# Kernel optimization log

Measured on AMD Instinct MI355X. Metric: run time of the kernel, lower is better.

The kernel has to match this reference:

```python
import jax, jax.numpy as jnp
import numpy as np

EMBED = 768
NH = 12          # num_heads
NL = 3           # num_levels
NP = 4           # num_points
DV = 384         # value dim = embed_dim * deform_ratio(0.5)
DH = DV // NH    # per-head value dim = 32
B = 16
LQ = 1024        # (512/16)^2 ViT tokens
SHAPES = [(64, 64), (32, 32), (16, 16)]  # 1/8, 1/16, 1/32 pyramid of 512x512
LKV = sum(h * w for h, w in SHAPES)      # 5376
EPS = 1e-6


def layer_norm(x, w, b):
    mu = jnp.mean(x, axis=-1, keepdims=True)
    var = jnp.mean((x - mu) ** 2, axis=-1, keepdims=True)
    return (x - mu) / jnp.sqrt(var + EPS) * w + b


def bilinear_sample(v, loc, H, W):
    # v: (B, NH, H*W, DH); loc: (B, Lq, NH, P, 2) normalized in [0,1]
    # Matches torch grid_sample(align_corners=False, padding_mode='zeros').
    Bv, Lq = loc.shape[0], loc.shape[1]
    x = loc[..., 0] * W - 0.5
    y = loc[..., 1] * H - 0.5
    x0 = jnp.floor(x)
    y0 = jnp.floor(y)
    dx = x - x0
    dy = y - y0
    x0i = x0.astype(jnp.int32)
    y0i = y0.astype(jnp.int32)

    def gather(xi, yi):
        valid = (xi >= 0) & (xi < W) & (yi >= 0) & (yi < H)  # (B,Lq,NH,P)
        xc = jnp.clip(xi, 0, W - 1)
        yc = jnp.clip(yi, 0, H - 1)
        lin = (yc * W + xc).transpose(0, 2, 1, 3).reshape(Bv, NH, Lq * NP)
        g = jnp.take_along_axis(v, lin[..., None], axis=2)  # (B,NH,Lq*P,DH)
        g = g.reshape(Bv, NH, Lq, NP, DH).transpose(0, 2, 1, 3, 4)  # (B,Lq,NH,P,DH)
        return g * valid[..., None].astype(g.dtype)

    g00 = gather(x0i, y0i)
    g01 = gather(x0i + 1, y0i)
    g10 = gather(x0i, y0i + 1)
    g11 = gather(x0i + 1, y0i + 1)
    w00 = ((1 - dx) * (1 - dy))[..., None]
    w01 = (dx * (1 - dy))[..., None]
    w10 = ((1 - dx) * dy)[..., None]
    w11 = (dx * dy)[..., None]
    return g00 * w00 + g01 * w01 + g10 * w10 + g11 * w11


def ms_deform_attn_core(value, shapes_list, loc, aw):
    # value: (B,LKV,NH,DH); loc: (B,Lq,NH,NL,NP,2); aw: (B,Lq,NH,NL,NP)
    Bv, Lq = loc.shape[0], loc.shape[1]
    samples = []
    idx = 0
    for l, (H, W) in enumerate(shapes_list):
        v = value[:, idx:idx + H * W].transpose(0, 2, 1, 3)  # (B,NH,HW,DH)
        idx += H * W
        samples.append(bilinear_sample(v, loc[:, :, :, l], H, W))
    s = jnp.stack(samples, axis=3)  # (B,Lq,NH,NL,NP,DH)
    o = jnp.einsum('bqhlp,bqhlpd->bqhd', aw, s)
    return o.reshape(Bv, Lq, NH * DH)


def setup_inputs() -> dict:
    key = jax.random.key(0)
    ks = jax.random.split(key, 12)

    def n(k, shape, s=0.02):
        return jax.random.normal(k, shape, jnp.float32) * s

    return {
        'q': jax.random.normal(ks[0], (B, LQ, EMBED), jnp.float32),
        'reference_points': jax.random.uniform(ks[1], (B, LQ, NL, 2), jnp.float32),
        'kv': jax.random.normal(ks[2], (B, LKV, EMBED), jnp.float32),
        'spatial_shapes': jnp.asarray(SHAPES, jnp.int32),
        'level_start_index': jnp.asarray(
            np.cumsum([0] + [h * w for h, w in SHAPES])[:-1], jnp.int32),
        'ln1_w': jnp.ones(EMBED, jnp.float32),
        'ln1_b': jnp.zeros(EMBED, jnp.float32),
        'ln2_w': jnp.ones(EMBED, jnp.float32),
        'ln2_b': jnp.zeros(EMBED, jnp.float32),
        'gamma': n(ks[3], (EMBED,), 0.1),
        'w_off': n(ks[4], (EMBED, NH * NL * NP * 2)),
        'b_off': n(ks[5], (NH * NL * NP * 2,), 0.01),
        'w_aw': n(ks[6], (EMBED, NH * NL * NP)),
        'b_aw': jnp.zeros(NH * NL * NP, jnp.float32),
        'w_val': n(ks[7], (EMBED, DV)),
        'b_val': jnp.zeros(DV, jnp.float32),
        'w_out': n(ks[8], (DV, EMBED)),
        'b_out': jnp.zeros(EMBED, jnp.float32),
    }


def reference(q, reference_points, kv, spatial_shapes, level_start_index,
              ln1_w, ln1_b, ln2_w, ln2_b, gamma,
              w_off, b_off, w_aw, b_aw, w_val, b_val, w_out, b_out):
    shapes_list = [tuple(int(v) for v in r) for r in np.asarray(spatial_shapes)]
    Bq, Lq, _ = q.shape
    qn = layer_norm(q, ln1_w, ln1_b)
    kvn = layer_norm(kv, ln2_w, ln2_b)
    value = (kvn @ w_val + b_val).reshape(Bq, -1, NH, DH)
    off = (qn @ w_off + b_off).reshape(Bq, Lq, NH, NL, NP, 2)
    aw = (qn @ w_aw + b_aw).reshape(Bq, Lq, NH, NL * NP)
    aw = jax.nn.softmax(aw, axis=-1).reshape(Bq, Lq, NH, NL, NP)
    # offset normalizer is (W_l, H_l) per level
    wh = jnp.asarray([[w, h] for (h, w) in shapes_list], q.dtype)  # (NL,2)
    loc = reference_points[:, :, None, :, None, :] + off / wh[None, None, None, :, None, :]
    attn = ms_deform_attn_core(value, shapes_list, loc, aw)
    attn = attn @ w_out + b_out
    return q + gamma * attn
```

## Files before the change

### kernel.cpp

```cpp
#include <hip/hip_runtime.h>

#define DEV __device__ __forceinline__

typedef short bf16x8 __attribute__((ext_vector_type(8)));
typedef float f32x4 __attribute__((ext_vector_type(4)));
typedef unsigned int u32;
typedef __attribute__((address_space(1))) const u32* gas_ptr;
typedef __attribute__((address_space(3))) u32* las_ptr;

DEV short f2bf(float f) {
  union { float f; unsigned u; } un; un.f = f;
  unsigned r = un.u + 0x7FFFu + ((un.u >> 16) & 1u);
  return (short)(r >> 16);
}
DEV float bf2f(unsigned short s) {
  union { unsigned u; float f; } un;
  un.u = ((unsigned)s) << 16;
  return un.f;
}
DEV void gload16(const short* g, short* l) {
  __builtin_amdgcn_global_load_lds((gas_ptr)g, (las_ptr)l, 16, 0, 0);
}

DEV float blockReduceSum256(float v, volatile float* sbuf) {
  #pragma unroll
  for (int off = 32; off > 0; off >>= 1) v += __shfl_down(v, off, 64);
  const int wv = threadIdx.x >> 6, ln = threadIdx.x & 63;
  if (ln == 0) sbuf[wv] = v;
  __syncthreads();
  return sbuf[0] + sbuf[1] + sbuf[2] + sbuf[3];
}

__global__ __launch_bounds__(256) void pack_weights_kernel(
    const float* __restrict__ w_val, const float* __restrict__ w_off,
    const float* __restrict__ w_aw, const float* __restrict__ w_out,
    const float* __restrict__ b_off, const float* __restrict__ b_aw,
    short* __restrict__ wT_val, short* __restrict__ wT_offaw,
    short* __restrict__ wT_out, float* __restrict__ bias_cat) {
  int gid = blockIdx.x * 256 + threadIdx.x;
  const int S0 = 768 * 384, S1 = 768 * 288, S2 = 768 * 144, S3 = 384 * 768;
  const int S4 = 16 * 768, S5 = 448;
  if (gid < S0) { int k = gid / 384, n = gid % 384; wT_val[n * 768 + k] = f2bf(w_val[gid]); return; }
  gid -= S0;
  if (gid < S1) { int k = gid / 288, n = gid % 288; wT_offaw[n * 768 + k] = f2bf(w_off[gid]); return; }
  gid -= S1;
  if (gid < S2) { int k = gid / 144, n = gid % 144; wT_offaw[(288 + n) * 768 + k] = f2bf(w_aw[gid]); return; }
  gid -= S2;
  if (gid < S3) { int k = gid / 768, n = gid % 768; wT_out[n * 384 + k] = f2bf(w_out[gid]); return; }
  gid -= S3;
  if (gid < S4) { wT_offaw[432 * 768 + gid] = 0; return; }
  gid -= S4;
  if (gid < S5) { bias_cat[gid] = (gid < 288) ? b_off[gid] : (gid < 432 ? b_aw[gid - 288] : 0.f); }
}

__global__ __launch_bounds__(256) void ln_norm_kernel(
    const float* __restrict__ x, const float* __restrict__ w,
    const float* __restrict__ b, short* __restrict__ y) {
  const int row = blockIdx.x;
  const float* xr = x + (size_t)row * 768;
  const int t = threadIdx.x;
  float a0 = xr[t], a1 = xr[t + 256], a2 = xr[t + 512];
  __shared__ float sb1[4], sb2[4];
  float mu = blockReduceSum256(a0 + a1 + a2, sb1) * (1.f / 768.f);
  float d0 = a0 - mu, d1 = a1 - mu, d2 = a2 - mu;
  float var = blockReduceSum256(d0 * d0 + d1 * d1 + d2 * d2, sb2) * (1.f / 768.f);
  const float rs = rsqrtf(var + 1e-6f);
  short* yr = y + (size_t)row * 768;
  yr[t]       = f2bf(d0 * rs * w[t]       + b[t]);
  yr[t + 256] = f2bf(d1 * rs * w[t + 256] + b[t + 256]);
  yr[t + 512] = f2bf(d2 * rs * w[t + 512] + b[t + 512]);
}

template <int EMODE>
__global__ __launch_bounds__(256, 3) void gemm128_kernel(
    const short* __restrict__ A, const short* __restrict__ Wt,
    const float* __restrict__ bias, const float* __restrict__ qres,
    const float* __restrict__ gamma, void* __restrict__ Cout,
    const int N, const int K) {
  __shared__ __align__(16) short As[128 * 32];
  __shared__ __align__(16) short Bs[128 * 32];
  const int tid = threadIdx.x;
  const int wave = tid >> 6, lane = tid & 63;
  const int n0 = blockIdx.x * 128, row0 = blockIdx.y * 128;
  const int lr = lane & 15, quad = lane >> 4;
  const int wm = wave >> 1, wn = wave & 1;

  const short* gA[2]; const short* gB[2];
  #pragma unroll
  for (int rnd = 0; rnd < 2; rnd++) {
    int G = rnd * 256 + wave * 64 + lane;
    int line = G >> 3, pos = G & 7, x = pos ^ (line & 7);
    int r = line * 2 + (x >> 2), qk = (x & 3) * 8;
    gA[rnd] = A + (size_t)(row0 + r) * K + qk;
    gB[rnd] = Wt + (size_t)(n0 + r) * K + qk;
  }
  short* ldsA[2] = {&As[(wave * 64) * 8], &As[(256 + wave * 64) * 8]};
  short* ldsB[2] = {&Bs[(wave * 64) * 8], &Bs[(256 + wave * 64) * 8]};

  const short* aF[4]; const short* bF[4];
  #pragma unroll
  for (int t4 = 0; t4 < 4; t4++) {
    int r = wm * 64 + t4 * 16 + lr;
    int line = r >> 1, pos = ((r & 1) * 4 + quad) ^ (line & 7);
    aF[t4] = &As[(line * 8 + pos) * 8];
    int rb = wn * 64 + t4 * 16 + lr;
    int lineb = rb >> 1, posb = ((rb & 1) * 4 + quad) ^ (lineb & 7);
    bF[t4] = &Bs[(lineb * 8 + posb) * 8];
  }

  f32x4 acc[4][4];
  #pragma unroll
  for (int i = 0; i < 4; i++)
    #pragma unroll
    for (int j = 0; j < 4; j++)
      #pragma unroll
      for (int e = 0; e < 4; e++) acc[i][j][e] = 0.f;

  for (int k0 = 0; k0 < K; k0 += 32) {
    gload16(gA[0], ldsA[0]);
    gload16(gA[1], ldsA[1]);
    gload16(gB[0], ldsB[0]);
    gload16(gB[1], ldsB[1]);
    gA[0] += 32; gA[1] += 32; gB[0] += 32; gB[1] += 32;
    __syncthreads();
    bf16x8 av[4], bv[4];
    #pragma unroll
    for (int t4 = 0; t4 < 4; t4++) {
      av[t4] = *(const bf16x8*)aF[t4];
      bv[t4] = *(const bf16x8*)bF[t4];
    }
    #pragma unroll
    for (int ct = 0; ct < 4; ct++)
      #pragma unroll
      for (int rt = 0; rt < 4; rt++)
        acc[rt][ct] = __builtin_amdgcn_mfma_f32_16x16x32_bf16(av[rt], bv[ct], acc[rt][ct], 0, 0, 0);
    __syncthreads();
  }

  #pragma unroll
  for (int ct = 0; ct < 4; ct++) {
    const int n = n0 + wn * 64 + ct * 16 + lr;
    const float bs = bias[n];
    const float gm = (EMODE == 2) ? gamma[n] : 0.f;
    #pragma unroll
    for (int rt = 0; rt < 4; rt++) {
      #pragma unroll
      for (int i = 0; i < 4; i++) {
        const int m = row0 + wm * 64 + rt * 16 + quad * 4 + i;
        float v = acc[rt][ct][i] + bs;
        if (EMODE == 0) {
          ((short*)Cout)[(size_t)m * N + n] = f2bf(v);
        } else {
          ((float*)Cout)[(size_t)m * N + n] = qres[(size_t)m * N + n] + gm * v;
        }
      }
    }
  }
}

template <int NT2>
__global__ __launch_bounds__(256, 2) void gemmw_kernel(
    const short* __restrict__ A, const short* __restrict__ Wt,
    const float* __restrict__ bias, float* __restrict__ Cout,
    const int N, const int K) {
  constexpr int BN = NT2 * 64;
  __shared__ __align__(16) short As[64 * 40];
  __shared__ __align__(16) short Bs[BN * 40];
  const int tid = threadIdx.x;
  const int wave = tid >> 6, lane = tid & 63;
  const int sr = tid >> 2;
  const int sk = (tid & 3) * 8;
  const int n0 = blockIdx.x * BN;
  const int row0 = blockIdx.y * 64;
  const int lr = lane & 15, quad = lane >> 4;

  f32x4 acc[4][NT2];
  #pragma unroll
  for (int rt = 0; rt < 4; rt++)
    #pragma unroll
    for (int cb = 0; cb < NT2; cb++)
      #pragma unroll
      for (int j = 0; j < 4; j++) acc[rt][cb][j] = 0.f;

  const short* AsF = &As[lr * 40 + quad * 8];
  const short* BsF = &Bs[(wave * NT2 * 16 + lr) * 40 + quad * 8];

  for (int k0 = 0; k0 < K; k0 += 32) {
    bf16x8 av = *(const bf16x8*)(A + (size_t)(row0 + sr) * K + k0 + sk);
    *(bf16x8*)(&As[sr * 40 + sk]) = av;
    #pragma unroll
    for (int i = tid; i < BN * 4; i += 256) {
      int n = i >> 2, kk = (i & 3) * 8;
      *(bf16x8*)(&Bs[n * 40 + kk]) =
          *(const bf16x8*)(Wt + (size_t)(n0 + n) * K + k0 + kk);
    }
    __syncthreads();
    bf16x8 af[4];
    #pragma unroll
    for (int rt = 0; rt < 4; rt++) af[rt] = *(const bf16x8*)(AsF + rt * 16 * 40);
    #pragma unroll
    for (int cb = 0; cb < NT2; cb++) {
      bf16x8 bfv = *(const bf16x8*)(BsF + cb * 16 * 40);
      #pragma unroll
      for (int rt = 0; rt < 4; rt++)
        acc[rt][cb] = __builtin_amdgcn_mfma_f32_16x16x32_bf16(af[rt], bfv, acc[rt][cb], 0, 0, 0);
    }
    __syncthreads();
  }

  #pragma unroll
  for (int cb = 0; cb < NT2; cb++) {
    const int n = n0 + wave * NT2 * 16 + cb * 16 + lr;
    const float bs = bias[n];
    #pragma unroll
    for (int rt = 0; rt < 4; rt++) {
      #pragma unroll
      for (int i = 0; i < 4; i++) {
        const int m = row0 + rt * 16 + quad * 4 + i;
        Cout[(size_t)m * N + n] = acc[rt][cb][i] + bs;
      }
    }
  }
}

__global__ __launch_bounds__(384) void sampler_kernel(
    const float* __restrict__ offaw,
    const float* __restrict__ refp,
    const short* __restrict__ value,
    short* __restrict__ o) {
  const int tid = threadIdx.x;
  const int qi = tid / 96, t = tid % 96;
  const int head = t >> 3, ln4 = t & 7;
  const int bq = blockIdx.x * 4 + qi;
  __shared__ __align__(16) float s[4][440];
  __shared__ float sref[4][6];
  const float* row = offaw + (size_t)bq * 448;
  #pragma unroll
  for (int i = t; i < 108; i += 96)
    *(float4*)&s[qi][i * 4] = *(const float4*)&row[i * 4];
  if (t < 6) sref[qi][t] = refp[(size_t)bq * 6 + t];
  __syncthreads();

  const float* awp = &s[qi][288 + head * 12];
  float mx = awp[0];
  #pragma unroll
  for (int j = 1; j < 12; j++) mx = fmaxf(mx, awp[j]);
  float wgt[12];
  float ssum = 0.f;
  #pragma unroll
  for (int j = 0; j < 12; j++) { float e = __expf(awp[j] - mx); wgt[j] = e; ssum += e; }
  const float inv = 1.f / ssum;

  const int b = bq >> 10;
  const unsigned short* vb =
      (const unsigned short*)value + (size_t)b * 5376 * 384 + head * 32 + ln4 * 4;
  float4 acc = make_float4(0.f, 0.f, 0.f, 0.f);
  const int HW[3] = {64, 32, 16};
  const int starts[3] = {0, 4096, 5120};
  #pragma unroll
  for (int l = 0; l < 3; l++) {
    const int Wi = HW[l];
    const float Wf = (float)Wi;
    const float rx = sref[qi][l * 2], ry = sref[qi][l * 2 + 1];
    const unsigned short* base = vb + (size_t)starts[l] * 384;
    #pragma unroll
    for (int p = 0; p < 4; p++) {
      const int oi = ((head * 3 + l) * 4 + p) * 2;
      float x = fmaf(rx, Wf, s[qi][oi] - 0.5f);
      float y = fmaf(ry, Wf, s[qi][oi + 1] - 0.5f);
      float xf = floorf(x), yf = floorf(y);
      float dx = x - xf, dy = y - yf;
      int x0 = (int)xf, y0 = (int)yf;
      int x1 = x0 + 1, y1 = y0 + 1;
      int x0c = min(max(x0, 0), Wi - 1), x1c = min(max(x1, 0), Wi - 1);
      int y0c = min(max(y0, 0), Wi - 1), y1c = min(max(y1, 0), Wi - 1);
      float wx0 = (x0 >= 0 && x0 < Wi) ? (1.f - dx) : 0.f;
      float wx1 = (x1 < Wi && x1 >= 0) ? dx : 0.f;
      float wy0 = (y0 >= 0 && y0 < Wi) ? (1.f - dy) : 0.f;
      float wy1 = (y1 < Wi && y1 >= 0) ? dy : 0.f;
      const ushort4 u00 = *(const ushort4*)(base + (size_t)(y0c * Wi + x0c) * 384);
      const ushort4 u01 = *(const ushort4*)(base + (size_t)(y0c * Wi + x1c) * 384);
      const ushort4 u10 = *(const ushort4*)(base + (size_t)(y1c * Wi + x0c) * 384);
      const ushort4 u11 = *(const ushort4*)(base + (size_t)(y1c * Wi + x1c) * 384);
      const float w00 = wx0 * wy0, w01 = wx1 * wy0, w10 = wx0 * wy1, w11 = wx1 * wy1;
      const float g = wgt[l * 4 + p];
      acc.x += g * (w00 * bf2f(u00.x) + w01 * bf2f(u01.x) + w10 * bf2f(u10.x) + w11 * bf2f(u11.x));
      acc.y += g * (w00 * bf2f(u00.y) + w01 * bf2f(u01.y) + w10 * bf2f(u10.y) + w11 * bf2f(u11.y));
      acc.z += g * (w00 * bf2f(u00.z) + w01 * bf2f(u01.z) + w10 * bf2f(u10.z) + w11 * bf2f(u11.z));
      acc.w += g * (w00 * bf2f(u00.w) + w01 * bf2f(u01.w) + w10 * bf2f(u10.w) + w11 * bf2f(u11.w));
    }
  }
  ushort4 outv;
  outv.x = (unsigned short)f2bf(acc.x * inv);
  outv.y = (unsigned short)f2bf(acc.y * inv);
  outv.z = (unsigned short)f2bf(acc.z * inv);
  outv.w = (unsigned short)f2bf(acc.w * inv);
  *(ushort4*)((unsigned short*)o + (size_t)bq * 384 + head * 32 + ln4 * 4) = outv;
}

extern "C" void kernel_launch(void* const* d_in, const int* in_sizes, int n_in,
                              void* d_out, int out_size, void* d_ws, size_t ws_size,
                              hipStream_t stream) {
  (void)in_sizes; (void)n_in; (void)out_size; (void)ws_size;
  const float* q     = (const float*)d_in[0];
  const float* refp  = (const float*)d_in[1];
  const float* kv    = (const float*)d_in[2];
  const float* ln1w  = (const float*)d_in[5];
  const float* ln1b  = (const float*)d_in[6];
  const float* ln2w  = (const float*)d_in[7];
  const float* ln2b  = (const float*)d_in[8];
  const float* gamma = (const float*)d_in[9];
  const float* w_off = (const float*)d_in[10];
  const float* b_off = (const float*)d_in[11];
  const float* w_aw  = (const float*)d_in[12];
  const float* b_aw  = (const float*)d_in[13];
  const float* w_val = (const float*)d_in[14];
  const float* b_val = (const float*)d_in[15];
  const float* w_out = (const float*)d_in[16];
  const float* b_out = (const float*)d_in[17];
  float* out = (float*)d_out;

  char* wsp = (char*)d_ws;
  size_t cur = 0;
  auto alloc = [&](size_t bytes) -> void* {
    cur = (cur + 255) & ~(size_t)255;
    void* p = wsp + cur;
    cur += bytes;
    return p;
  };
  short*  wT_val   = (short*)alloc((size_t)384 * 768 * 2);
  short*  wT_offaw = (short*)alloc((size_t)448 * 768 * 2);
  short*  wT_out   = (short*)alloc((size_t)768 * 384 * 2);
  float*  bias_cat = (float*)alloc((size_t)448 * 4);
  short*  kvn      = (short*)alloc((size_t)86016 * 768 * 2);
  short*  qn       = (short*)alloc((size_t)16384 * 768 * 2);
  short*  value    = (short*)alloc((size_t)86016 * 384 * 2);
  float*  offaw    = (float*)alloc((size_t)16384 * 448 * 4);
  short*  obuf     = (short*)alloc((size_t)16384 * 384 * 2);

  pack_weights_kernel<<<3651, 256, 0, stream>>>(w_val, w_off, w_aw, w_out, b_off,
                                                b_aw, wT_val, wT_offaw, wT_out,
                                                bias_cat);
  ln_norm_kernel<<<86016, 256, 0, stream>>>(kv, ln2w, ln2b, kvn);
  ln_norm_kernel<<<16384, 256, 0, stream>>>(q, ln1w, ln1b, qn);
  gemm128_kernel<0><<<dim3(3, 672), 256, 0, stream>>>(
      kvn, wT_val, b_val, nullptr, nullptr, value, 384, 768);
  gemmw_kernel<7><<<dim3(1, 256), 256, 0, stream>>>(
      qn, wT_offaw, bias_cat, offaw, 448, 768);
  sampler_kernel<<<4096, 384, 0, stream>>>(offaw, refp, value, obuf);
  gemm128_kernel<2><<<dim3(6, 128), 256, 0, stream>>>(
      obuf, wT_out, b_out, q, gamma, out, 768, 384);
}
```

Measured before the change: 735.9 us.

## Use wave-per-row LayerNorm, swizzle GEMM blocks, pad offaw GEMM to 512 columns

LayerNorm now gives each row to a single wave, loading with float4 and reducing with xor shuffles, which removes the LDS round trips and block barriers. The GEMM kernel remaps block IDs into 8 interleaved groups so neighbouring blocks land on different XCDs or caches. The offset/attention-weight projection is padded from 448 to 512 columns so it can reuse the 128x128 GEMM in place of the separate narrow-tile kernel. The padding adds some wasted MFMA work and a larger intermediate buffer.

```diff
diff --git a/kernel.cpp b/kernel.cpp
--- a/kernel.cpp
+++ b/kernel.cpp
@@ -21,15 +21,7 @@
 DEV void gload16(const short* g, short* l) {
   __builtin_amdgcn_global_load_lds((gas_ptr)g, (las_ptr)l, 16, 0, 0);
 }
-
-DEV float blockReduceSum256(float v, volatile float* sbuf) {
-  #pragma unroll
-  for (int off = 32; off > 0; off >>= 1) v += __shfl_down(v, off, 64);
-  const int wv = threadIdx.x >> 6, ln = threadIdx.x & 63;
-  if (ln == 0) sbuf[wv] = v;
-  __syncthreads();
-  return sbuf[0] + sbuf[1] + sbuf[2] + sbuf[3];
-}
+DEV float hsum4(float4 v) { return v.x + v.y + v.z + v.w; }
 
 __global__ __launch_bounds__(256) void pack_weights_kernel(
     const float* __restrict__ w_val, const float* __restrict__ w_off,
@@ -39,7 +31,7 @@
     short* __restrict__ wT_out, float* __restrict__ bias_cat) {
   int gid = blockIdx.x * 256 + threadIdx.x;
   const int S0 = 768 * 384, S1 = 768 * 288, S2 = 768 * 144, S3 = 384 * 768;
-  const int S4 = 16 * 768, S5 = 448;
+  const int S4 = 80 * 768, S5 = 512;
   if (gid < S0) { int k = gid / 384, n = gid % 384; wT_val[n * 768 + k] = f2bf(w_val[gid]); return; }
   gid -= S0;
   if (gid < S1) { int k = gid / 288, n = gid % 288; wT_offaw[n * 768 + k] = f2bf(w_off[gid]); return; }
@@ -53,22 +45,51 @@
   if (gid < S5) { bias_cat[gid] = (gid < 288) ? b_off[gid] : (gid < 432 ? b_aw[gid - 288] : 0.f); }
 }
 
-__global__ __launch_bounds__(256) void ln_norm_kernel(
+__global__ __launch_bounds__(256) void ln_norm4_kernel(
     const float* __restrict__ x, const float* __restrict__ w,
     const float* __restrict__ b, short* __restrict__ y) {
-  const int row = blockIdx.x;
+  const int wv = threadIdx.x >> 6, lane = threadIdx.x & 63;
+  const int row = blockIdx.x * 4 + wv;
   const float* xr = x + (size_t)row * 768;
-  const int t = threadIdx.x;
-  float a0 = xr[t], a1 = xr[t + 256], a2 = xr[t + 512];
-  __shared__ float sb1[4], sb2[4];
-  float mu = blockReduceSum256(a0 + a1 + a2, sb1) * (1.f / 768.f);
-  float d0 = a0 - mu, d1 = a1 - mu, d2 = a2 - mu;
-  float var = blockReduceSum256(d0 * d0 + d1 * d1 + d2 * d2, sb2) * (1.f / 768.f);
-  const float rs = rsqrtf(var + 1e-6f);
-  short* yr = y + (size_t)row * 768;
-  yr[t]       = f2bf(d0 * rs * w[t]       + b[t]);
-  yr[t + 256] = f2bf(d1 * rs * w[t + 256] + b[t + 256]);
-  yr[t + 512] = f2bf(d2 * rs * w[t + 512] + b[t + 512]);
+  float4 v0 = *(const float4*)(xr + lane * 4);
+  float4 v1 = *(const float4*)(xr + 256 + lane * 4);
+  float4 v2 = *(const float4*)(xr + 512 + lane * 4);
+  float s = hsum4(v0) + hsum4(v1) + hsum4(v2);
+  #pragma unroll
+  for (int off = 32; off > 0; off >>= 1) s += __shfl_xor(s, off, 64);
+  const float mu = s * (1.f / 768.f);
+  float4 d0 = make_float4(v0.x - mu, v0.y - mu, v0.z - mu, v0.w - mu);
+  float4 d1 = make_float4(v1.x - mu, v1.y - mu, v1.z - mu, v1.w - mu);
+  float4 d2 = make_float4(v2.x - mu, v2.y - mu, v2.z - mu, v2.w - mu);
+  float vs = d0.x * d0.x + d0.y * d0.y + d0.z * d0.z + d0.w * d0.w +
+             d1.x * d1.x + d1.y * d1.y + d1.z * d1.z + d1.w * d1.w +
+             d2.x * d2.x + d2.y * d2.y + d2.z * d2.z + d2.w * d2.w;
+  #pragma unroll
+  for (int off = 32; off > 0; off >>= 1) vs += __shfl_xor(vs, off, 64);
+  const float rs = rsqrtf(vs * (1.f / 768.f) + 1e-6f);
+  const float4 w0 = *(const float4*)(w + lane * 4);
+  const float4 w1 = *(const float4*)(w + 256 + lane * 4);
+  const float4 w2 = *(const float4*)(w + 512 + lane * 4);
+  const float4 b0 = *(const float4*)(b + lane * 4);
+  const float4 b1 = *(const float4*)(b + 256 + lane * 4);
+  const float4 b2 = *(const float4*)(b + 512 + lane * 4);
+  unsigned short* yr = (unsigned short*)y + (size_t)row * 768;
+  ushort4 o;
+  o.x = (unsigned short)f2bf(d0.x * rs * w0.x + b0.x);
+  o.y = (unsigned short)f2bf(d0.y * rs * w0.y + b0.y);
+  o.z = (unsigned short)f2bf(d0.z * rs * w0.z + b0.z);
+  o.w = (unsigned short)f2bf(d0.w * rs * w0.w + b0.w);
+  *(ushort4*)(yr + lane * 4) = o;
+  o.x = (unsigned short)f2bf(d1.x * rs * w1.x + b1.x);
+  o.y = (unsigned short)f2bf(d1.y * rs * w1.y + b1.y);
+  o.z = (unsigned short)f2bf(d1.z * rs * w1.z + b1.z);
+  o.w = (unsigned short)f2bf(d1.w * rs * w1.w + b1.w);
+  *(ushort4*)(yr + 256 + lane * 4) = o;
+  o.x = (unsigned short)f2bf(d2.x * rs * w2.x + b2.x);
+  o.y = (unsigned short)f2bf(d2.y * rs * w2.y + b2.y);
+  o.z = (unsigned short)f2bf(d2.z * rs * w2.z + b2.z);
+  o.w = (unsigned short)f2bf(d2.w * rs * w2.w + b2.w);
+  *(ushort4*)(yr + 512 + lane * 4) = o;
 }
 
 template <int EMODE>
@@ -81,7 +102,13 @@
   __shared__ __align__(16) short Bs[128 * 32];
   const int tid = threadIdx.x;
   const int wave = tid >> 6, lane = tid & 63;
-  const int n0 = blockIdx.x * 128, row0 = blockIdx.y * 128;
+
+  const int nx = gridDim.x;
+  const int id = blockIdx.y * nx + blockIdx.x;
+  const int cpx = (nx * gridDim.y) >> 3;
+  const int swz = (id & 7) * cpx + (id >> 3);
+  const int n0 = (swz % nx) * 128, row0 = (swz / nx) * 128;
+
   const int lr = lane & 15, quad = lane >> 4;
   const int wm = wave >> 1, wn = wave & 1;
 
@@ -150,74 +177,11 @@
         float v = acc[rt][ct][i] + bs;
         if (EMODE == 0) {
           ((short*)Cout)[(size_t)m * N + n] = f2bf(v);
+        } else if (EMODE == 1) {
+          ((float*)Cout)[(size_t)m * N + n] = v;
         } else {
           ((float*)Cout)[(size_t)m * N + n] = qres[(size_t)m * N + n] + gm * v;
         }
-      }
-    }
-  }
-}
-
-template <int NT2>
-__global__ __launch_bounds__(256, 2) void gemmw_kernel(
-    const short* __restrict__ A, const short* __restrict__ Wt,
-    const float* __restrict__ bias, float* __restrict__ Cout,
-    const int N, const int K) {
-  constexpr int BN = NT2 * 64;
-  __shared__ __align__(16) short As[64 * 40];
-  __shared__ __align__(16) short Bs[BN * 40];
-  const int tid = threadIdx.x;
-  const int wave = tid >> 6, lane = tid & 63;
-  const int sr = tid >> 2;
-  const int sk = (tid & 3) * 8;
-  const int n0 = blockIdx.x * BN;
-  const int row0 = blockIdx.y * 64;
-  const int lr = lane & 15, quad = lane >> 4;
-
-  f32x4 acc[4][NT2];
-  #pragma unroll
-  for (int rt = 0; rt < 4; rt++)
-    #pragma unroll
-    for (int cb = 0; cb < NT2; cb++)
-      #pragma unroll
-      for (int j = 0; j < 4; j++) acc[rt][cb][j] = 0.f;
-
-  const short* AsF = &As[lr * 40 + quad * 8];
-  const short* BsF = &Bs[(wave * NT2 * 16 + lr) * 40 + quad * 8];
-
-  for (int k0 = 0; k0 < K; k0 += 32) {
-    bf16x8 av = *(const bf16x8*)(A + (size_t)(row0 + sr) * K + k0 + sk);
-    *(bf16x8*)(&As[sr * 40 + sk]) = av;
-    #pragma unroll
-    for (int i = tid; i < BN * 4; i += 256) {
-      int n = i >> 2, kk = (i & 3) * 8;
-      *(bf16x8*)(&Bs[n * 40 + kk]) =
-          *(const bf16x8*)(Wt + (size_t)(n0 + n) * K + k0 + kk);
-    }
-    __syncthreads();
-    bf16x8 af[4];
-    #pragma unroll
-    for (int rt = 0; rt < 4; rt++) af[rt] = *(const bf16x8*)(AsF + rt * 16 * 40);
-    #pragma unroll
-    for (int cb = 0; cb < NT2; cb++) {
-      bf16x8 bfv = *(const bf16x8*)(BsF + cb * 16 * 40);
-      #pragma unroll
-      for (int rt = 0; rt < 4; rt++)
-        acc[rt][cb] = __builtin_amdgcn_mfma_f32_16x16x32_bf16(af[rt], bfv, acc[rt][cb], 0, 0, 0);
-    }
-    __syncthreads();
-  }
-
-  #pragma unroll
-  for (int cb = 0; cb < NT2; cb++) {
-    const int n = n0 + wave * NT2 * 16 + cb * 16 + lr;
-    const float bs = bias[n];
-    #pragma unroll
-    for (int rt = 0; rt < 4; rt++) {
-      #pragma unroll
-      for (int i = 0; i < 4; i++) {
-        const int m = row0 + rt * 16 + quad * 4 + i;
-        Cout[(size_t)m * N + n] = acc[rt][cb][i] + bs;
       }
     }
   }
@@ -234,7 +198,7 @@
   const int bq = blockIdx.x * 4 + qi;
   __shared__ __align__(16) float s[4][440];
   __shared__ float sref[4][6];
-  const float* row = offaw + (size_t)bq * 448;
+  const float* row = offaw + (size_t)bq * 512;
   #pragma unroll
   for (int i = t; i < 108; i += 96)
     *(float4*)&s[qi][i * 4] = *(const float4*)&row[i * 4];
@@ -329,24 +293,24 @@
     return p;
   };
   short*  wT_val   = (short*)alloc((size_t)384 * 768 * 2);
-  short*  wT_offaw = (short*)alloc((size_t)448 * 768 * 2);
+  short*  wT_offaw = (short*)alloc((size_t)512 * 768 * 2);
   short*  wT_out   = (short*)alloc((size_t)768 * 384 * 2);
-  float*  bias_cat = (float*)alloc((size_t)448 * 4);
+  float*  bias_cat = (float*)alloc((size_t)512 * 4);
   short*  kvn      = (short*)alloc((size_t)86016 * 768 * 2);
   short*  qn       = (short*)alloc((size_t)16384 * 768 * 2);
   short*  value    = (short*)alloc((size_t)86016 * 384 * 2);
-  float*  offaw    = (float*)alloc((size_t)16384 * 448 * 4);
+  float*  offaw    = (float*)alloc((size_t)16384 * 512 * 4);
   short*  obuf     = (short*)alloc((size_t)16384 * 384 * 2);
 
-  pack_weights_kernel<<<3651, 256, 0, stream>>>(w_val, w_off, w_aw, w_out, b_off,
+  pack_weights_kernel<<<3842, 256, 0, stream>>>(w_val, w_off, w_aw, w_out, b_off,
                                                 b_aw, wT_val, wT_offaw, wT_out,
                                                 bias_cat);
-  ln_norm_kernel<<<86016, 256, 0, stream>>>(kv, ln2w, ln2b, kvn);
-  ln_norm_kernel<<<16384, 256, 0, stream>>>(q, ln1w, ln1b, qn);
+  ln_norm4_kernel<<<21504, 256, 0, stream>>>(kv, ln2w, ln2b, kvn);
+  ln_norm4_kernel<<<4096, 256, 0, stream>>>(q, ln1w, ln1b, qn);
   gemm128_kernel<0><<<dim3(3, 672), 256, 0, stream>>>(
       kvn, wT_val, b_val, nullptr, nullptr, value, 384, 768);
-  gemmw_kernel<7><<<dim3(1, 256), 256, 0, stream>>>(
-      qn, wT_offaw, bias_cat, offaw, 448, 768);
+  gemm128_kernel<1><<<dim3(4, 128), 256, 0, stream>>>(
+      qn, wT_offaw, bias_cat, nullptr, nullptr, offaw, 512, 768);
   sampler_kernel<<<4096, 384, 0, stream>>>(offaw, refp, value, obuf);
   gemm128_kernel<2><<<dim3(6, 128), 256, 0, stream>>>(
       obuf, wT_out, b_out, q, gamma, out, 768, 384);
```

After: 665.8 us. 1.11x faster.
